# Performance work log

Measured on AMD Instinct MI355X. Metric: run time of the kernel, lower is better.

## Reference

```python
import jax, jax.numpy as jnp
import numpy as np

# Soft boolean gates on {0,1} float pulses (exact boolean algebra on 0/1 inputs)
def _and(a, b):
    return a * b

def _or(a, b):
    return a + b - a * b

def _xor(a, b):
    return a + b - 2.0 * a * b

def _not(a):
    return 1.0 - a

def _mux(sel, a, b):
    return sel * a + (1.0 - sel) * b

def _or_reduce(x):
    # OR-chain over last axis == 1 - prod(1-x) for 0/1 bits
    return 1.0 - jnp.prod(1.0 - x, axis=-1, keepdims=True)

def _and_reduce(x):
    return jnp.prod(x, axis=-1, keepdims=True)

def _sub_lsb(A, B, n):
    """A - B over n bits, LSB first; returns (diff_bits, borrow_out)."""
    borrow = jnp.zeros_like(A[..., 0:1])
    diffs = []
    for i in range(n):  # fixed 8-iter borrow chain (structural, not data dim)
        a = A[..., i:i + 1]
        b = B[..., i:i + 1]
        diff = _xor(_xor(a, b), borrow)
        na = _not(a)
        borrow = _or(_or(_and(na, b), _and(na, borrow)), _and(b, borrow))
        diffs.append(diff)
    return jnp.concatenate(diffs, axis=-1), borrow

def _add_lsb(A, B, n):
    """A + B over n bits, LSB first; returns (sum_bits, carry_out)."""
    carry = jnp.zeros_like(A[..., 0:1])
    sums = []
    for i in range(n):  # fixed-width ripple carry (<=11 iters)
        a = A[..., i:i + 1]
        b = B[..., i:i + 1]
        axb = _xor(a, b)
        sums.append(_xor(axb, carry))
        carry = _or(_and(a, b), _and(carry, axb))
    return jnp.concatenate(sums, axis=-1), carry

def _cmp_msb(A, B, n):
    """N-bit comparator, MSB first; returns (A>B, A==B) as 0/1 bits."""
    xor_all = _xor(A, B)
    eq_all = _not(xor_all)
    gt_all = _and(A, _not(B))
    a_eq_b = _and_reduce(eq_all)
    eq_prefix = eq_all[..., 0:1]
    a_gt_b = gt_all[..., 0:1]
    for i in range(1, n):
        a_gt_b = _or(a_gt_b, _and(eq_prefix, gt_all[..., i:i + 1]))
        if i < n - 1:
            eq_prefix = _and(eq_prefix, eq_all[..., i:i + 1])
    return a_gt_b, a_eq_b

def _const_bits(bits, like):
    c = jnp.asarray(bits, dtype=like.dtype)
    return jnp.broadcast_to(c, like.shape[:-1] + (len(bits),))


def setup_inputs() -> dict:
    key = jax.random.key(0)
    bits = jax.random.randint(key, (2048, 1024, 32), 0, 2)
    return {"fp32_pulse": bits.astype(jnp.float32)}


def reference(fp32_pulse) -> jnp.ndarray:
    zeros = jnp.zeros_like(fp32_pulse[..., 0:1])
    ones = jnp.ones_like(zeros)

    s = fp32_pulse[..., 0:1]
    fp32_exp = fp32_pulse[..., 1:9]      # 8 exponent bits, MSB first
    fp32_mant = fp32_pulse[..., 9:32]    # 23 mantissa bits, MSB first

    # special-value detection
    e_all_one = _and_reduce(fp32_exp)
    m_any_one = _or_reduce(fp32_mant)
    is_nan = _and(e_all_one, m_any_one)
    is_inf = _and(e_all_one, _not(m_any_one))

    # exponent rebias: fp16_exp = fp32_exp - 112 (LSB-first subtractor)
    fp32_exp_lsb = jnp.flip(fp32_exp, axis=-1)
    const_112_lsb = _const_bits([0, 0, 0, 0, 1, 1, 1, 0], zeros)
    fp16_exp_raw_lsb, _ = _sub_lsb(fp32_exp_lsb, const_112_lsb, 8)
    fp16_exp_lsb = fp16_exp_raw_lsb[..., :5]
    fp16_exp = jnp.flip(fp16_exp_lsb, axis=-1)

    # overflow: fp32_exp > 142 ; underflow: 113 > fp32_exp (MSB-first comparators)
    const_142 = _const_bits([1, 0, 0, 0, 1, 1, 1, 0], zeros)
    const_113 = _const_bits([0, 1, 1, 1, 0, 0, 0, 1], zeros)
    is_overflow, _ = _cmp_msb(fp32_exp, const_142, 8)
    is_underflow, _ = _cmp_msb(const_113, fp32_exp, 8)

    # mantissa truncation + RNE rounding
    fp16_mant_raw = fp32_mant[..., :10]
    L = fp32_mant[..., 9:10]
    R = fp32_mant[..., 10:11]
    S = _or_reduce(fp32_mant[..., 11:23])  # sticky = OR of bits 11..22
    round_up = _and(R, _or(S, L))

    fp16_mant_lsb = jnp.flip(fp16_mant_raw, axis=-1)
    mant_11bit_lsb = jnp.concatenate([fp16_mant_lsb, zeros], axis=-1)
    round_inc_lsb = jnp.concatenate([round_up] + [zeros] * 10, axis=-1)
    mant_rounded_lsb, _ = _add_lsb(mant_11bit_lsb, round_inc_lsb, 11)
    mant_carry = mant_rounded_lsb[..., 10:11]
    fp16_mant = jnp.flip(mant_rounded_lsb[..., :10], axis=-1)

    # if rounding carried out, clear mantissa and bump exponent
    not_carry = _not(mant_carry)
    fp16_mant_final = _and(not_carry, fp16_mant)

    exp_inc_lsb = jnp.concatenate([mant_carry, zeros, zeros, zeros, zeros], axis=-1)
    exp_after_round_lsb, _ = _add_lsb(fp16_exp_lsb, exp_inc_lsb, 5)
    exp_after_round = jnp.flip(exp_after_round_lsb, axis=-1)
    final_exp = _mux(mant_carry, exp_after_round, fp16_exp)

    result = jnp.concatenate([s, final_exp, fp16_mant_final], axis=-1)

    nan_val = jnp.concatenate([s] + [ones] * 6 + [zeros] * 9, axis=-1)
    inf_val = jnp.concatenate([s] + [ones] * 5 + [zeros] * 10, axis=-1)
    zero_val = jnp.concatenate([zeros] * 16, axis=-1)

    # special-case muxes, applied in original order
    result = _mux(is_overflow, inf_val, result)
    result = _mux(is_underflow, zero_val, result)
    result = _mux(is_inf, inf_val, result)
    result = _mux(is_nan, nan_val, result)
    return result
```

## Files before the change

kernel.cpp:

```cpp
#include <hip/hip_runtime.h>


__global__ __launch_bounds__(256) void fp32_to_fp16_bits_kernel(
    const float* __restrict__ in, float* __restrict__ out, int n_elems)
{
    int e = blockIdx.x * blockDim.x + threadIdx.x;
    if (e >= n_elems) return;

    const float4* in4 = reinterpret_cast<const float4*>(in) + (size_t)e * 8;
    uint32_t bits = 0u;
#pragma unroll
    for (int k = 0; k < 8; ++k) {
        float4 v = in4[k];
        uint32_t b0 = (v.x != 0.0f) ? 1u : 0u;
        uint32_t b1 = (v.y != 0.0f) ? 1u : 0u;
        uint32_t b2 = (v.z != 0.0f) ? 1u : 0u;
        uint32_t b3 = (v.w != 0.0f) ? 1u : 0u;
        int sh = 31 - 4 * k;
        bits |= (b0 << sh) | (b1 << (sh - 1)) | (b2 << (sh - 2)) | (b3 << (sh - 3));
    }

    uint32_t s = bits >> 31;
    uint32_t E = (bits >> 23) & 0xFFu;
    uint32_t M = bits & 0x7FFFFFu;

    uint32_t mant10   = M >> 13;
    uint32_t L        = mant10 & 1u;
    uint32_t R        = (M >> 12) & 1u;
    uint32_t S        = ((M & 0xFFFu) != 0u) ? 1u : 0u;
    uint32_t round_up = R & (L | S);

    uint32_t mr       = mant10 + round_up;
    uint32_t carry    = mr >> 10;
    uint32_t mant_out = mr & 0x3FFu;

    uint32_t exp5 = (E - 112u + carry) & 0x1Fu;

    uint32_t h = (s << 15) | (exp5 << 10) | mant_out;

    bool e_all = (E == 0xFFu);
    bool m_any = (M != 0u);
    if (E > 142u)        h = (s << 15) | 0x7C00u;
    if (E < 113u)        h = 0u;
    if (e_all && !m_any) h = (s << 15) | 0x7C00u;
    if (e_all &&  m_any) h = (s << 15) | 0x7E00u;

    float4* o4 = reinterpret_cast<float4*>(out) + (size_t)e * 4;
#pragma unroll
    for (int k = 0; k < 4; ++k) {
        int sh = 15 - 4 * k;
        float4 v;
        v.x = (float)((h >> sh) & 1u);
        v.y = (float)((h >> (sh - 1)) & 1u);
        v.z = (float)((h >> (sh - 2)) & 1u);
        v.w = (float)((h >> (sh - 3)) & 1u);
        o4[k] = v;
    }
}

extern "C" void kernel_launch(void* const* d_in, const int* in_sizes, int n_in,
                              void* d_out, int out_size, void* d_ws, size_t ws_size,
                              hipStream_t stream) {
    const float* in = (const float*)d_in[0];
    float* out = (float*)d_out;
    int n_elems = in_sizes[0] / 32;
    int block = 256;
    int grid = (n_elems + block - 1) / block;
    fp32_to_fp16_bits_kernel<<<grid, block, 0, stream>>>(in, out, n_elems);
}
```

Before: 391.3 us.

## Coalesce loads and stores via wave ballots and shuffles

Each 64-lane wavefront now reads its 64 elements' input as contiguous float4s across lanes, not a 128-byte strided chunk per thread. Bits are gathered with __ballot and redistributed to the owning lane with shifts, spread and bit-reverse. Output is written the same coalesced way, using __shfl to fetch each element's fp16 bits. This adds cross-lane ballot and shuffle work and assumes a wavefront size of 64 and n_elems divisible by 64.

```diff
diff --git a/kernel.cpp b/kernel.cpp
--- a/kernel.cpp
+++ b/kernel.cpp
@@ -1,24 +1,48 @@
 #include <hip/hip_runtime.h>
 
+
+__device__ __forceinline__ uint32_t spread4(uint32_t x) {
+    x &= 0xFFu;
+    x = (x | (x << 12)) & 0x000F000Fu;
+    x = (x | (x << 6))  & 0x03030303u;
+    x = (x | (x << 3))  & 0x11111111u;
+    return x;
+}
 
 __global__ __launch_bounds__(256) void fp32_to_fp16_bits_kernel(
     const float* __restrict__ in, float* __restrict__ out, int n_elems)
 {
-    int e = blockIdx.x * blockDim.x + threadIdx.x;
-    if (e >= n_elems) return;
+    int tid  = blockIdx.x * blockDim.x + threadIdx.x;
+    int lane = threadIdx.x & 63;
+    long elemBase = (long)(tid >> 6) * 64;
+    if (elemBase >= n_elems) return;
 
-    const float4* in4 = reinterpret_cast<const float4*>(in) + (size_t)e * 8;
-    uint32_t bits = 0u;
+    const float4* in4 = reinterpret_cast<const float4*>(in) + elemBase * 8;
+
+    float4 v[8];
 #pragma unroll
-    for (int k = 0; k < 8; ++k) {
-        float4 v = in4[k];
-        uint32_t b0 = (v.x != 0.0f) ? 1u : 0u;
-        uint32_t b1 = (v.y != 0.0f) ? 1u : 0u;
-        uint32_t b2 = (v.z != 0.0f) ? 1u : 0u;
-        uint32_t b3 = (v.w != 0.0f) ? 1u : 0u;
-        int sh = 31 - 4 * k;
-        bits |= (b0 << sh) | (b1 << (sh - 1)) | (b2 << (sh - 2)) | (b3 << (sh - 3));
+    for (int j = 0; j < 8; ++j) v[j] = in4[j * 64 + lane];
+
+    unsigned long long z0 = 0, z1 = 0, z2 = 0, z3 = 0;
+#pragma unroll
+    for (int j = 0; j < 8; ++j) {
+        unsigned long long b0 = __ballot(v[j].x != 0.0f);
+        unsigned long long b1 = __ballot(v[j].y != 0.0f);
+        unsigned long long b2 = __ballot(v[j].z != 0.0f);
+        unsigned long long b3 = __ballot(v[j].w != 0.0f);
+        if ((lane >> 3) == j) { z0 = b0; z1 = b1; z2 = b2; z3 = b3; }
     }
+
+    int shb = (lane & 7) << 3;
+    uint32_t B0 = (uint32_t)(z0 >> shb) & 0xFFu;
+    uint32_t B1 = (uint32_t)(z1 >> shb) & 0xFFu;
+    uint32_t B2 = (uint32_t)(z2 >> shb) & 0xFFu;
+    uint32_t B3 = (uint32_t)(z3 >> shb) & 0xFFu;
+
+    uint32_t bits = (__brev(spread4(B0))     )
+                  | (__brev(spread4(B1)) >> 1)
+                  | (__brev(spread4(B2)) >> 2)
+                  | (__brev(spread4(B3)) >> 3);
 
     uint32_t s = bits >> 31;
     uint32_t E = (bits >> 23) & 0xFFu;
@@ -33,8 +57,7 @@
     uint32_t mr       = mant10 + round_up;
     uint32_t carry    = mr >> 10;
     uint32_t mant_out = mr & 0x3FFu;
-
-    uint32_t exp5 = (E - 112u + carry) & 0x1Fu;
+    uint32_t exp5     = (E - 112u + carry) & 0x1Fu;
 
     uint32_t h = (s << 15) | (exp5 << 10) | mant_out;
 
@@ -45,16 +68,18 @@
     if (e_all && !m_any) h = (s << 15) | 0x7C00u;
     if (e_all &&  m_any) h = (s << 15) | 0x7E00u;
 
-    float4* o4 = reinterpret_cast<float4*>(out) + (size_t)e * 4;
+    float4* o4 = reinterpret_cast<float4*>(out) + elemBase * 4;
 #pragma unroll
     for (int k = 0; k < 4; ++k) {
-        int sh = 15 - 4 * k;
-        float4 v;
-        v.x = (float)((h >> sh) & 1u);
-        v.y = (float)((h >> (sh - 1)) & 1u);
-        v.z = (float)((h >> (sh - 2)) & 1u);
-        v.w = (float)((h >> (sh - 3)) & 1u);
-        o4[k] = v;
+        int src = 16 * k + (lane >> 2);
+        uint32_t hh = (uint32_t)__shfl((int)h, src, 64);
+        int base = 15 - 4 * (lane & 3);
+        float4 o;
+        o.x = (float)((hh >> base)       & 1u);
+        o.y = (float)((hh >> (base - 1)) & 1u);
+        o.z = (float)((hh >> (base - 2)) & 1u);
+        o.w = (float)((hh >> (base - 3)) & 1u);
+        o4[k * 64 + lane] = o;
     }
 }
 
```

After: 386.2 us. About the same (-1.3%).
